# Performance work log

Hardware: AMD Instinct MI355X
Metric: run time of the kernel (lower is better)

Reference implementation:

```python
import jax, jax.numpy as jnp
import numpy as np

N, E, F_IN, HID, L, G = 50000, 800000, 128, 64, 3, 512
BN_EPS = 1e-5


def setup_inputs() -> dict:
    key = jax.random.key(0)
    ks = jax.random.split(key, 8)
    x = jax.random.normal(ks[0], (N, F_IN), dtype=jnp.float32)
    edge_index = jax.random.randint(ks[1], (2, E), 0, N, dtype=jnp.int32)
    batch = jnp.sort(jax.random.randint(ks[2], (N,), 0, G, dtype=jnp.int32))
    # params (Glorot-ish init for weights; BN init per module: gamma=1, beta=1e-4)
    W_feat = jax.random.normal(ks[3], (F_IN, HID), dtype=jnp.float32) / np.sqrt(F_IN)
    b_feat = jnp.zeros((HID,), jnp.float32)
    Ws = jax.random.normal(ks[4], (L, HID, HID), dtype=jnp.float32) / np.sqrt(HID)
    bs = jnp.zeros((L, HID), jnp.float32)
    bn_feat_g = jnp.ones((F_IN,), jnp.float32)
    bn_feat_b = jnp.full((F_IN,), 1e-4, jnp.float32)
    bn_g = jnp.ones((L, HID), jnp.float32)
    bn_b = jnp.full((L, HID), 1e-4, jnp.float32)
    return {"x": x, "edge_index": edge_index, "batch": batch,
            "bn_feat_g": bn_feat_g, "bn_feat_b": bn_feat_b,
            "W_feat": W_feat, "b_feat": b_feat,
            "bn_g": bn_g, "bn_b": bn_b, "Ws": Ws, "bs": bs}


def batch_norm(x, gamma, beta):
    # training-mode BatchNorm1d: biased variance over the node dimension
    mu = jnp.mean(x, axis=0)
    var = jnp.mean(jnp.square(x - mu), axis=0)
    return (x - mu) * jax.lax.rsqrt(var + BN_EPS) * gamma + beta


def gcn_conv(h, W, b, src, dst):
    # h: [N, d_in] -> linear then normalized gather-scatter with self-loops
    h = h @ W  # [N, d_out]
    n = h.shape[0]
    loop = jnp.arange(n, dtype=src.dtype)
    row = jnp.concatenate([src, loop])  # source (j)
    col = jnp.concatenate([dst, loop])  # target (i)
    w = jnp.ones(row.shape[0], h.dtype)
    deg = jax.ops.segment_sum(w, row, num_segments=n)  # PyG: deg over row
    dis = jnp.where(deg > 0, jax.lax.rsqrt(jnp.maximum(deg, 1.0)), 0.0)
    norm = dis[row] * w * dis[col]  # [E+N]
    out = jax.ops.segment_sum(norm[:, None] * h[row], col, num_segments=n)
    return out + b


def reference(x, edge_index, batch, bn_feat_g, bn_feat_b, W_feat, b_feat,
              bn_g, bn_b, Ws, bs):
    src, dst = edge_index[0], edge_index[1]
    h = batch_norm(x, bn_feat_g, bn_feat_b)
    h = jax.nn.relu(h @ W_feat + b_feat)  # conv_feat has gfn=True -> plain linear
    for i in range(L):
        h = batch_norm(h, bn_g[i], bn_b[i])
        h = jax.nn.relu(gcn_conv(h, Ws[i], bs[i], src, dst))
    graph_emb = jax.ops.segment_sum(h, batch, num_segments=G)  # global_add_pool
    return graph_emb
```

## Files before the change

kernel.cpp:

```cpp
#include <hip/hip_runtime.h>
#include <math.h>

#define HID 64
#define BN_EPS 1e-5f
#define NREP 64

typedef unsigned int uint;
typedef unsigned short ushort;


__device__ inline uint bf16pk(float a, float b) {
    uint ua = __builtin_bit_cast(uint, a);
    ua += 0x7fff + ((ua >> 16) & 1);
    uint ub = __builtin_bit_cast(uint, b);
    ub += 0x7fff + ((ub >> 16) & 1);
    return (ua >> 16) | (ub & 0xffff0000u);
}
__device__ inline float bfl(uint v) { return __builtin_bit_cast(float, v << 16); }
__device__ inline float bfh(uint v) { return __builtin_bit_cast(float, v & 0xffff0000u); }


__global__ __launch_bounds__(256) void k_hist_scan_stats(
        const int* __restrict__ ei, int E, int NB, int N, int HB,
        int* __restrict__ bcnt_d, int* __restrict__ bcnt_s, int* __restrict__ done,
        int* __restrict__ bbase_d, int* __restrict__ cursor_d,
        int* __restrict__ bbase_s, int* __restrict__ cursor_s,
        int* __restrict__ rowptr,
        const float* __restrict__ X, int n, float* __restrict__ stats) {
    __shared__ __align__(16) char smemraw[8192];
    __shared__ int lastFlag;
    int t = threadIdx.x;
    if ((int)blockIdx.x < HB) {
        int* hd = (int*)smemraw;
        int* hs = hd + 256;
        hd[t] = 0; hs[t] = 0;
        __syncthreads();
        for (int e = blockIdx.x * 256 + t; e < E; e += HB * 256) {
            int src = ei[e], dst = ei[E + e];
            atomicAdd(&hs[src >> 8], 1);
            atomicAdd(&hd[dst >> 8], 1);
        }
        __syncthreads();
        if (t < NB) {
            if (hd[t]) atomicAdd(&bcnt_d[t], hd[t]);
            if (hs[t]) atomicAdd(&bcnt_s[t], hs[t]);
        }
        __threadfence();
        __syncthreads();
        if (t == 0) lastFlag = (atomicAdd(done, 1) == HB - 1);
        __syncthreads();
        if (!lastFlag) return;
        int v = (t < NB) ? atomicAdd(&bcnt_d[t], 0) : 0;
        hd[t] = v; __syncthreads();
        for (int s = 1; s < 256; s <<= 1) { int u = (t >= s) ? hd[t - s] : 0; __syncthreads(); hd[t] += u; __syncthreads(); }
        int excl = hd[t] - v;
        if (t <= NB) bbase_d[t] = excl;
        if (t < NB) cursor_d[t] = excl;
        if (t == 0) rowptr[N] = E;
        __syncthreads();
        v = (t < NB) ? atomicAdd(&bcnt_s[t], 0) : 0;
        hs[t] = v; __syncthreads();
        for (int s = 1; s < 256; s <<= 1) { int u = (t >= s) ? hs[t - s] : 0; __syncthreads(); hs[t] += u; __syncthreads(); }
        excl = hs[t] - v;
        if (t <= NB) bbase_s[t] = excl;
        if (t < NB) cursor_s[t] = excl;
    } else {
        int b = blockIdx.x - HB;
        int SB = gridDim.x - HB;
        float4* shs = (float4*)smemraw;
        float4* shq = shs + 256;
        int c4 = t & 31, rsub = t >> 5;
        float4 s = make_float4(0.f, 0.f, 0.f, 0.f);
        float4 q = make_float4(0.f, 0.f, 0.f, 0.f);
        for (int r = b * 8 + rsub; r < n; r += SB * 8) {
            float4 v = ((const float4*)X)[(size_t)r * 32 + c4];
            s.x += v.x; s.y += v.y; s.z += v.z; s.w += v.w;
            q.x = fmaf(v.x, v.x, q.x); q.y = fmaf(v.y, v.y, q.y);
            q.z = fmaf(v.z, v.z, q.z); q.w = fmaf(v.w, v.w, q.w);
        }
        shs[t] = s; shq[t] = q;
        __syncthreads();
        if (rsub == 0) {
            #pragma unroll
            for (int k = 1; k < 8; k++) {
                float4 a = shs[t + k * 32], bq = shq[t + k * 32];
                s.x += a.x; s.y += a.y; s.z += a.z; s.w += a.w;
                q.x += bq.x; q.y += bq.y; q.z += bq.z; q.w += bq.w;
            }
            float* sb = stats + ((int)blockIdx.x & (NREP - 1)) * 256;
            atomicAdd(&sb[4 * t + 0], s.x); atomicAdd(&sb[4 * t + 1], s.y);
            atomicAdd(&sb[4 * t + 2], s.z); atomicAdd(&sb[4 * t + 3], s.w);
            atomicAdd(&sb[128 + 4 * t + 0], q.x); atomicAdd(&sb[128 + 4 * t + 1], q.y);
            atomicAdd(&sb[128 + 4 * t + 2], q.z); atomicAdd(&sb[128 + 4 * t + 3], q.w);
        }
    }
}


template <int K, bool RELU, bool DIS, bool STATS, bool HASB>
__device__ __forceinline__ void gemm_body(const float* __restrict__ X, const float* __restrict__ W,
                                          const float* __restrict__ stats,
                                          const float* __restrict__ gamma, const float* __restrict__ beta,
                                          const float* __restrict__ bias0, const float* __restrict__ dis,
                                          float n_inv, void* __restrict__ out, int n,
                                          float* __restrict__ sout, int bx) {
    constexpr int KC = 64;
    constexpr int XS = 68;
    __shared__ float Xs[KC * XS];
    __shared__ float Wsm[KC * HID];
    __shared__ float As[128], Cs[128];

    int t = threadIdx.x;
    int tx = t & 15, ty = t >> 4;
    int row0 = bx * 64;

    if (t < K) {
        float ssum = 0.f, qsum = 0.f;
        const float* sp = stats + t;
        #pragma unroll 8
        for (int r = 0; r < NREP; ++r) {
            ssum += sp[(size_t)r * 2 * K];
            qsum += sp[(size_t)r * 2 * K + K];
        }
        float mu = ssum * n_inv;
        float var = qsum * n_inv - mu * mu;
        float a = gamma[t] * rsqrtf(var + BN_EPS);
        As[t] = a;
        Cs[t] = beta[t] - mu * a;
    }
    __syncthreads();

    float acc[4][4];
    #pragma unroll
    for (int i = 0; i < 4; i++)
        #pragma unroll
        for (int j = 0; j < 4; j++) acc[i][j] = 0.f;
    float4 bp = make_float4(0.f, 0.f, 0.f, 0.f);

    for (int kc = 0; kc < K; kc += KC) {
        #pragma unroll
        for (int it = 0; it < 4; ++it) {
            int id = t + 256 * it;
            int r = id >> 4, c4 = id & 15;
            float4 v = make_float4(0.f, 0.f, 0.f, 0.f);
            if (row0 + r < n) v = *(const float4*)(X + (size_t)(row0 + r) * K + kc + 4 * c4);
            int kk = 4 * c4;
            Xs[(kk + 0) * XS + r] = v.x;
            Xs[(kk + 1) * XS + r] = v.y;
            Xs[(kk + 2) * XS + r] = v.z;
            Xs[(kk + 3) * XS + r] = v.w;
        }
        {
            const float4* wsrc = (const float4*)(W + (size_t)kc * HID);
            #pragma unroll
            for (int it = 0; it < 4; ++it) {
                int id = t + 256 * it;
                int kl = id >> 4;
                float4 raw = wsrc[id];
                float a = As[kc + kl], c = Cs[kc + kl];
                float4 sc;
                sc.x = a * raw.x; sc.y = a * raw.y; sc.z = a * raw.z; sc.w = a * raw.w;
                ((float4*)Wsm)[id] = sc;
                bp.x = fmaf(c, raw.x, bp.x);
                bp.y = fmaf(c, raw.y, bp.y);
                bp.z = fmaf(c, raw.z, bp.z);
                bp.w = fmaf(c, raw.w, bp.w);
            }
        }
        __syncthreads();
        #pragma unroll 8
        for (int k = 0; k < KC; ++k) {
            float4 xv = *(const float4*)&Xs[k * XS + 4 * ty];
            float4 wv = *(const float4*)&Wsm[k * HID + 4 * tx];
            acc[0][0] = fmaf(xv.x, wv.x, acc[0][0]);
            acc[0][1] = fmaf(xv.x, wv.y, acc[0][1]);
            acc[0][2] = fmaf(xv.x, wv.z, acc[0][2]);
            acc[0][3] = fmaf(xv.x, wv.w, acc[0][3]);
            acc[1][0] = fmaf(xv.y, wv.x, acc[1][0]);
            acc[1][1] = fmaf(xv.y, wv.y, acc[1][1]);
            acc[1][2] = fmaf(xv.y, wv.z, acc[1][2]);
            acc[1][3] = fmaf(xv.y, wv.w, acc[1][3]);
            acc[2][0] = fmaf(xv.z, wv.x, acc[2][0]);
            acc[2][1] = fmaf(xv.z, wv.y, acc[2][1]);
            acc[2][2] = fmaf(xv.z, wv.z, acc[2][2]);
            acc[2][3] = fmaf(xv.z, wv.w, acc[2][3]);
            acc[3][0] = fmaf(xv.w, wv.x, acc[3][0]);
            acc[3][1] = fmaf(xv.w, wv.y, acc[3][1]);
            acc[3][2] = fmaf(xv.w, wv.z, acc[3][2]);
            acc[3][3] = fmaf(xv.w, wv.w, acc[3][3]);
        }
        __syncthreads();
    }

    {
        float* redb = Xs + 2048;
        *(float4*)&redb[ty * 64 + 4 * tx] = bp;
        __syncthreads();
        if (t < 64) {
            float s = 0.f;
            #pragma unroll
            for (int k = 0; k < 16; ++k) s += redb[k * 64 + t];
            Xs[3072 + t] = s + (HASB ? bias0[t] : 0.f);
        }
        __syncthreads();
    }
    float4 bv = *(const float4*)&Xs[3072 + 4 * tx];

    float4 cs = make_float4(0.f, 0.f, 0.f, 0.f);
    float4 cq = make_float4(0.f, 0.f, 0.f, 0.f);
    #pragma unroll
    for (int i = 0; i < 4; ++i) {
        int row = row0 + 4 * ty + i;
        bool valid = row < n;
        float vx = acc[i][0] + bv.x, vy = acc[i][1] + bv.y;
        float vz = acc[i][2] + bv.z, vw = acc[i][3] + bv.w;
        if constexpr (DIS) {
            if (valid) {
                float d = dis[row];
                uint2 pk;
                pk.x = bf16pk(vx * d, vy * d);
                pk.y = bf16pk(vz * d, vw * d);
                *(uint2*)((ushort*)out + (size_t)row * HID + 4 * tx) = pk;
            }
        } else {
            float4 v;
            v.x = RELU ? fmaxf(vx, 0.f) : vx;
            v.y = RELU ? fmaxf(vy, 0.f) : vy;
            v.z = RELU ? fmaxf(vz, 0.f) : vz;
            v.w = RELU ? fmaxf(vw, 0.f) : vw;
            if (valid) {
                *(float4*)((float*)out + (size_t)row * HID + 4 * tx) = v;
                if constexpr (STATS) {
                    cs.x += v.x; cs.y += v.y; cs.z += v.z; cs.w += v.w;
                    cq.x = fmaf(v.x, v.x, cq.x); cq.y = fmaf(v.y, v.y, cq.y);
                    cq.z = fmaf(v.z, v.z, cq.z); cq.w = fmaf(v.w, v.w, cq.w);
                }
            }
        }
    }
    if constexpr (STATS) {
        __syncthreads();
        float* reds = Xs;
        float* redq = Xs + 1024;
        *(float4*)&reds[ty * 64 + 4 * tx] = cs;
        *(float4*)&redq[ty * 64 + 4 * tx] = cq;
        __syncthreads();
        if (t < 64) {
            float s = 0.f, q = 0.f;
            #pragma unroll
            for (int k = 0; k < 16; ++k) { s += reds[k * 64 + t]; q += redq[k * 64 + t]; }
            float* sb = sout + ((int)bx & (NREP - 1)) * 128;
            atomicAdd(&sb[t], s);
            atomicAdd(&sb[64 + t], q);
        }
    }
}

template <int K, bool RELU, bool DIS, bool STATS, bool HASB>
__global__ __launch_bounds__(256) void k_gemm(const float* __restrict__ X, const float* __restrict__ W,
                                              const float* __restrict__ stats,
                                              const float* __restrict__ gamma, const float* __restrict__ beta,
                                              const float* __restrict__ bias0, const float* __restrict__ dis,
                                              float n_inv, void* __restrict__ out, int n,
                                              float* __restrict__ sout) {
    gemm_body<K, RELU, DIS, STATS, HASB>(X, W, stats, gamma, beta, bias0, dis, n_inv, out, n, sout,
                                         (int)blockIdx.x);
}


__global__ __launch_bounds__(256) void k_scatter_gemm(
        const int* __restrict__ ei, int E, int NB, int SCB,
        int* __restrict__ cursor_d, int* __restrict__ cursor_s,
        uint* __restrict__ bedge, int* __restrict__ bsrc,
        const float* __restrict__ X, const float* __restrict__ W,
        const float* __restrict__ stats,
        const float* __restrict__ gamma, const float* __restrict__ beta,
        const float* __restrict__ bias0,
        float n_inv, void* __restrict__ out, int n, float* __restrict__ sout) {
    int t = threadIdx.x;
    if ((int)blockIdx.x < SCB) {
        __shared__ int hd[256], hs[256], curd[256], curs[256];
        int chunk = (E + SCB - 1) / SCB;
        int e0 = blockIdx.x * chunk;
        int e1 = min(e0 + chunk, E);
        if (t < NB) { hd[t] = 0; hs[t] = 0; }
        __syncthreads();
        for (int e = e0 + t; e < e1; e += 256) {
            int src = ei[e], dst = ei[E + e];
            atomicAdd(&hd[dst >> 8], 1);
            atomicAdd(&hs[src >> 8], 1);
        }
        __syncthreads();
        if (t < NB) {
            curd[t] = hd[t] ? atomicAdd(&cursor_d[t], hd[t]) : 0;
            curs[t] = hs[t] ? atomicAdd(&cursor_s[t], hs[t]) : 0;
        }
        __syncthreads();
        for (int e = e0 + t; e < e1; e += 256) {
            int src = ei[e], dst = ei[E + e];
            int pd = atomicAdd(&curd[dst >> 8], 1);
            bedge[pd] = ((uint)(dst & 255) << 16) | (uint)src;
            int ps = atomicAdd(&curs[src >> 8], 1);
            bsrc[ps] = src;
        }
    } else {
        gemm_body<128, true, false, true, true>(X, W, stats, gamma, beta, bias0, nullptr,
                                                n_inv, out, n, sout, (int)blockIdx.x - SCB);
    }
}


__global__ __launch_bounds__(256) void k_build_csr_outdeg(
        const uint* __restrict__ bedge, const int* __restrict__ bbase_d,
        const int* __restrict__ bsrc, const int* __restrict__ bbase_s,
        int N, int NB,
        int* __restrict__ rowptr, int* __restrict__ eidx, float* __restrict__ dis) {
    __shared__ int h[256], off[256], cur[256];
    int t = threadIdx.x, b = blockIdx.x;
    if (b < NB) {
        int base = bbase_d[b], end = bbase_d[b + 1];
        h[t] = 0; __syncthreads();
        for (int p = base + t; p < end; p += 256)
            atomicAdd(&h[(int)(bedge[p] >> 16) & 255], 1);
        __syncthreads();
        off[t] = h[t]; __syncthreads();
        for (int s = 1; s < 256; s <<= 1) { int u = (t >= s) ? off[t - s] : 0; __syncthreads(); off[t] += u; __syncthreads(); }
        int excl = off[t] - h[t];
        int node = (b << 8) + t;
        if (node <= N) rowptr[node] = base + excl;
        cur[t] = excl; __syncthreads();
        for (int p = base + t; p < end; p += 256) {
            uint be = bedge[p];
            int bin = (int)(be >> 16) & 255;
            int pos = atomicAdd(&cur[bin], 1);
            eidx[base + pos] = (int)(be & 0xffffu);
        }
    } else {
        int b2 = b - NB;
        int base = bbase_s[b2], end = bbase_s[b2 + 1];
        h[t] = 0; __syncthreads();
        for (int p = base + t; p < end; p += 256) atomicAdd(&h[bsrc[p] & 255], 1);
        __syncthreads();
        int node = (b2 << 8) + t;
        if (node < N) dis[node] = rsqrtf((float)(h[t] + 1));
    }
}


template <bool POOL>
__global__ __launch_bounds__(256) void k_agg(const ushort* __restrict__ s, const int* __restrict__ rowptr,
                                             const int* __restrict__ eidx, const float* __restrict__ dis,
                                             const float* __restrict__ bias, float* __restrict__ out, int n,
                                             float* __restrict__ sout, const int* __restrict__ batch,
                                             float* __restrict__ pool_out) {
    __shared__ float shs[8 * 64];
    __shared__ float shq[8 * 64];
    __shared__ int ib[8];
    int t = threadIdx.x;
    int nl = t >> 5;
    int li = t & 31;
    int slot = li >> 3;
    int c = li & 7;
    int i = blockIdx.x * 8 + nl;
    const uint4* sp4 = (const uint4*)s;
    float a[8];
    #pragma unroll
    for (int k = 0; k < 8; ++k) a[k] = 0.f;
    bool valid = i < n;
    if (valid) {
        int qe = rowptr[i + 1];
        int q = rowptr[i] + slot;
        while (q < qe) {
            int qm = qe - 1;
            int q1 = q + 4, q2 = q + 8, q3 = q + 12;
            bool p1 = q1 < qe, p2 = q2 < qe, p3 = q3 < qe;
            int j0 = eidx[q];
            int j1 = eidx[min(q1, qm)];
            int j2 = eidx[min(q2, qm)];
            int j3 = eidx[min(q3, qm)];
            if (!p1) j1 = i;
            if (!p2) j2 = i;
            if (!p3) j3 = i;
            uint4 v0 = sp4[(size_t)j0 * 8 + c];
            uint4 v1 = sp4[(size_t)j1 * 8 + c];
            uint4 v2 = sp4[(size_t)j2 * 8 + c];
            uint4 v3 = sp4[(size_t)j3 * 8 + c];
            float m1 = p1 ? 1.f : 0.f;
            float m2 = p2 ? 1.f : 0.f;
            float m3 = p3 ? 1.f : 0.f;
            q += 16;
            a[0] += bfl(v0.x); a[1] += bfh(v0.x);
            a[2] += bfl(v0.y); a[3] += bfh(v0.y);
            a[4] += bfl(v0.z); a[5] += bfh(v0.z);
            a[6] += bfl(v0.w); a[7] += bfh(v0.w);
            a[0] = fmaf(m1, bfl(v1.x), a[0]); a[1] = fmaf(m1, bfh(v1.x), a[1]);
            a[2] = fmaf(m1, bfl(v1.y), a[2]); a[3] = fmaf(m1, bfh(v1.y), a[3]);
            a[4] = fmaf(m1, bfl(v1.z), a[4]); a[5] = fmaf(m1, bfh(v1.z), a[5]);
            a[6] = fmaf(m1, bfl(v1.w), a[6]); a[7] = fmaf(m1, bfh(v1.w), a[7]);
            a[0] = fmaf(m2, bfl(v2.x), a[0]); a[1] = fmaf(m2, bfh(v2.x), a[1]);
            a[2] = fmaf(m2, bfl(v2.y), a[2]); a[3] = fmaf(m2, bfh(v2.y), a[3]);
            a[4] = fmaf(m2, bfl(v2.z), a[4]); a[5] = fmaf(m2, bfh(v2.z), a[5]);
            a[6] = fmaf(m2, bfl(v2.w), a[6]); a[7] = fmaf(m2, bfh(v2.w), a[7]);
            a[0] = fmaf(m3, bfl(v3.x), a[0]); a[1] = fmaf(m3, bfh(v3.x), a[1]);
            a[2] = fmaf(m3, bfl(v3.y), a[2]); a[3] = fmaf(m3, bfh(v3.y), a[3]);
            a[4] = fmaf(m3, bfl(v3.z), a[4]); a[5] = fmaf(m3, bfh(v3.z), a[5]);
            a[6] = fmaf(m3, bfl(v3.w), a[6]); a[7] = fmaf(m3, bfh(v3.w), a[7]);
        }
    }
    #pragma unroll
    for (int k = 0; k < 8; ++k) a[k] += __shfl_xor(a[k], 8);
    #pragma unroll
    for (int k = 0; k < 8; ++k) a[k] += __shfl_xor(a[k], 16);

    if (li < 8) {
        float r[8];
        if (valid) {
            uint4 v = sp4[(size_t)i * 8 + c];
            a[0] += bfl(v.x); a[1] += bfh(v.x);
            a[2] += bfl(v.y); a[3] += bfh(v.y);
            a[4] += bfl(v.z); a[5] += bfh(v.z);
            a[6] += bfl(v.w); a[7] += bfh(v.w);
            float d = dis[i];
            float4 b0 = *(const float4*)(bias + 8 * c);
            float4 b1 = *(const float4*)(bias + 8 * c + 4);
            r[0] = fmaxf(fmaf(d, a[0], b0.x), 0.f);
            r[1] = fmaxf(fmaf(d, a[1], b0.y), 0.f);
            r[2] = fmaxf(fmaf(d, a[2], b0.z), 0.f);
            r[3] = fmaxf(fmaf(d, a[3], b0.w), 0.f);
            r[4] = fmaxf(fmaf(d, a[4], b1.x), 0.f);
            r[5] = fmaxf(fmaf(d, a[5], b1.y), 0.f);
            r[6] = fmaxf(fmaf(d, a[6], b1.z), 0.f);
            r[7] = fmaxf(fmaf(d, a[7], b1.w), 0.f);
            if constexpr (!POOL) {
                *(float4*)(out + (size_t)i * HID + 8 * c)     = make_float4(r[0], r[1], r[2], r[3]);
                *(float4*)(out + (size_t)i * HID + 8 * c + 4) = make_float4(r[4], r[5], r[6], r[7]);
            }
        } else {
            #pragma unroll
            for (int k = 0; k < 8; ++k) r[k] = 0.f;
        }
        #pragma unroll
        for (int k = 0; k < 8; ++k) shs[nl * 64 + 8 * c + k] = r[k];
        if constexpr (!POOL) {
            #pragma unroll
            for (int k = 0; k < 8; ++k) shq[nl * 64 + 8 * c + k] = r[k] * r[k];
        }
    }
    if constexpr (POOL) {
        if (li == 0) ib[nl] = valid ? batch[i] : -1;
    }
    __syncthreads();
    if (t < 64) {
        if constexpr (!POOL) {
            float ss = 0.f, qq = 0.f;
            #pragma unroll
            for (int k = 0; k < 8; ++k) { ss += shs[k * 64 + t]; qq += shq[k * 64 + t]; }
            float* sb = sout + ((int)blockIdx.x & (NREP - 1)) * 128;
            atomicAdd(&sb[t], ss);
            atomicAdd(&sb[64 + t], qq);
        } else {
            int g = ib[0];
            float run = shs[t];
            #pragma unroll
            for (int k = 1; k < 8; ++k) {
                int gk = ib[k];
                float v = shs[k * 64 + t];
                if (gk == g) {
                    run += v;
                } else {
                    if (g >= 0) atomicAdd(&pool_out[(size_t)g * HID + t], run);
                    g = gk; run = v;
                }
            }
            if (g >= 0) atomicAdd(&pool_out[(size_t)g * HID + t], run);
        }
    }
}


extern "C" void kernel_launch(void* const* d_in, const int* in_sizes, int n_in,
                              void* d_out, int out_size, void* d_ws, size_t ws_size,
                              hipStream_t stream) {
    const float* x     = (const float*)d_in[0];
    const int*   ei    = (const int*)d_in[1];
    const int*   batch = (const int*)d_in[2];
    const float* bnfg  = (const float*)d_in[3];
    const float* bnfb  = (const float*)d_in[4];
    const float* Wfeat = (const float*)d_in[5];
    const float* bfeat = (const float*)d_in[6];
    const float* bng   = (const float*)d_in[7];
    const float* bnb   = (const float*)d_in[8];
    const float* Ws    = (const float*)d_in[9];
    const float* bs    = (const float*)d_in[10];
    float* out = (float*)d_out;

    const int N   = in_sizes[2];
    const int E   = in_sizes[1] / 2;
    const int L   = in_sizes[9] / (HID * HID);
    const int NB  = (N + 255) >> 8;
    const int HB  = 128;
    const int SB  = 512;
    const int SCB = 256;
    const int gG  = (N + 63) / 64;
    const int gA  = (N + 7) / 8;
    const float n_inv = 1.f / (float)N;

    char* w = (char*)d_ws;
    auto alloc = [&](size_t bytes) { char* p = w; w += (bytes + 255) & ~(size_t)255; return p; };
    int*   bcnt_d = (int*)alloc(256 * 4);
    int*   bcnt_s = (int*)alloc(256 * 4);
    int*   done   = (int*)alloc(256);
    float* statsX = (float*)alloc((size_t)NREP * 256 * 4);
    float* statsL = (float*)alloc((size_t)3 * NREP * 128 * 4);
    size_t zero_bytes = (size_t)(w - (char*)d_ws);
    int*   bbase_d  = (int*)alloc(257 * 4);
    int*   cursor_d = (int*)alloc(256 * 4);
    int*   bbase_s  = (int*)alloc(257 * 4);
    int*   cursor_s = (int*)alloc(256 * 4);
    int*   rowptr   = (int*)alloc(((size_t)N + 1) * 4);
    int*   eidx     = (int*)alloc((size_t)E * 4);
    float* dis      = (float*)alloc((size_t)N * 4);
    float* bufA     = (float*)alloc((size_t)N * HID * 4);
    ushort* bufB    = (ushort*)alloc((size_t)N * HID * 2);
    uint*  bedge    = (uint*)alloc((size_t)E * 4);
    int*   bsrc     = (int*)alloc((size_t)E * 4);

    hipMemsetAsync(d_ws, 0, zero_bytes, stream);
    hipMemsetAsync(d_out, 0, (size_t)out_size * sizeof(float), stream);

    k_hist_scan_stats<<<HB + SB, 256, 0, stream>>>(ei, E, NB, N, HB, bcnt_d, bcnt_s, done,
                                                   bbase_d, cursor_d, bbase_s, cursor_s, rowptr,
                                                   x, N, statsX);
    k_scatter_gemm<<<SCB + gG, 256, 0, stream>>>(ei, E, NB, SCB, cursor_d, cursor_s, bedge, bsrc,
                                                 x, Wfeat, statsX, bnfg, bnfb, bfeat,
                                                 n_inv, (void*)bufA, N, statsL);
    k_build_csr_outdeg<<<2 * NB, 256, 0, stream>>>(bedge, bbase_d, bsrc, bbase_s, N, NB,
                                                   rowptr, eidx, dis);

    for (int l = 0; l < L; ++l) {
        k_gemm<64, false, true, false, false><<<gG, 256, 0, stream>>>(
            bufA, Ws + (size_t)l * HID * HID, statsL + (size_t)l * NREP * 128,
            bng + (size_t)l * HID, bnb + (size_t)l * HID,
            nullptr, dis, n_inv, (void*)bufB, N, nullptr);
        if (l < L - 1) {
            k_agg<false><<<gA, 256, 0, stream>>>(bufB, rowptr, eidx, dis, bs + (size_t)l * HID,
                                                 bufA, N, statsL + (size_t)(l + 1) * NREP * 128,
                                                 nullptr, nullptr);
        } else {
            k_agg<true><<<gA, 256, 0, stream>>>(bufB, rowptr, eidx, dis, bs + (size_t)l * HID,
                                                nullptr, N, nullptr, batch, out);
        }
    }
}
```

Measured before the change: 260.4 us.

## Fuse CSR fill with first-layer GEMM and parallelize BN stats reduction

Splits the out-degree computation into its own kernel and merges the CSR fill with the layer-0 GEMM in one launch, so the two independent pieces of work run as different block ranges of the same grid. It also spreads the per-feature BN stat reduction across all 256 threads with a shared-memory combine step, where previously only K threads did it. The aim is to cut one serialized launch boundary and shorten the stats prologue of every GEMM, at the cost of an extra small kernel and a barrier.

After: 251.4 us. 1.04x faster.

```diff
diff --git a/kernel.cpp b/kernel.cpp
--- a/kernel.cpp
+++ b/kernel.cpp
@@ -106,6 +106,7 @@
                                           float* __restrict__ sout, int bx) {
     constexpr int KC = 64;
     constexpr int XS = 68;
+    constexpr int NSUB = 256 / K;
     __shared__ float Xs[KC * XS];
     __shared__ float Wsm[KC * HID];
     __shared__ float As[128], Cs[128];
@@ -114,16 +115,26 @@
     int tx = t & 15, ty = t >> 4;
     int row0 = bx * 64;
 
-    if (t < K) {
+    {
+        int f = t & (K - 1);
+        int sub = t / K;
         float ssum = 0.f, qsum = 0.f;
-        const float* sp = stats + t;
-        #pragma unroll 8
-        for (int r = 0; r < NREP; ++r) {
+        const float* sp = stats + f;
+        #pragma unroll 4
+        for (int r = sub; r < NREP; r += NSUB) {
             ssum += sp[(size_t)r * 2 * K];
             qsum += sp[(size_t)r * 2 * K + K];
         }
-        float mu = ssum * n_inv;
-        float var = qsum * n_inv - mu * mu;
+        Xs[t] = ssum;
+        Xs[256 + t] = qsum;
+    }
+    __syncthreads();
+    if (t < K) {
+        float ss = 0.f, qq = 0.f;
+        #pragma unroll
+        for (int s = 0; s < NSUB; ++s) { ss += Xs[s * K + t]; qq += Xs[256 + s * K + t]; }
+        float mu = ss * n_inv;
+        float var = qq * n_inv - mu * mu;
         float a = gamma[t] * rsqrtf(var + BN_EPS);
         As[t] = a;
         Cs[t] = beta[t] - mu * a;
@@ -249,7 +260,7 @@
             float s = 0.f, q = 0.f;
             #pragma unroll
             for (int k = 0; k < 16; ++k) { s += reds[k * 64 + t]; q += redq[k * 64 + t]; }
-            float* sb = sout + ((int)bx & (NREP - 1)) * 128;
+            float* sb = sout + (bx & (NREP - 1)) * 128;
             atomicAdd(&sb[t], s);
             atomicAdd(&sb[64 + t], q);
         }
@@ -310,14 +321,30 @@
 }
 
 
-__global__ __launch_bounds__(256) void k_build_csr_outdeg(
-        const uint* __restrict__ bedge, const int* __restrict__ bbase_d,
-        const int* __restrict__ bsrc, const int* __restrict__ bbase_s,
-        int N, int NB,
-        int* __restrict__ rowptr, int* __restrict__ eidx, float* __restrict__ dis) {
-    __shared__ int h[256], off[256], cur[256];
+__global__ __launch_bounds__(256) void k_dis(const int* __restrict__ bsrc, const int* __restrict__ bbase_s,
+                                             int N, float* __restrict__ dis) {
+    __shared__ int h[256];
+    int t = threadIdx.x, b = blockIdx.x;
+    int base = bbase_s[b], end = bbase_s[b + 1];
+    h[t] = 0; __syncthreads();
+    for (int p = base + t; p < end; p += 256) atomicAdd(&h[bsrc[p] & 255], 1);
+    __syncthreads();
+    int node = (b << 8) + t;
+    if (node < N) dis[node] = rsqrtf((float)(h[t] + 1));
+}
+
+
+__global__ __launch_bounds__(256) void k_fill_gemm(
+        const uint* __restrict__ bedge, const int* __restrict__ bbase_d, int N, int NB,
+        int* __restrict__ rowptr, int* __restrict__ eidx,
+        const float* __restrict__ X, const float* __restrict__ W,
+        const float* __restrict__ stats,
+        const float* __restrict__ gamma, const float* __restrict__ beta,
+        const float* __restrict__ dis,
+        float n_inv, void* __restrict__ out, int n) {
     int t = threadIdx.x, b = blockIdx.x;
     if (b < NB) {
+        __shared__ int h[256], off[256], cur[256];
         int base = bbase_d[b], end = bbase_d[b + 1];
         h[t] = 0; __syncthreads();
         for (int p = base + t; p < end; p += 256)
@@ -336,13 +363,8 @@
             eidx[base + pos] = (int)(be & 0xffffu);
         }
     } else {
-        int b2 = b - NB;
-        int base = bbase_s[b2], end = bbase_s[b2 + 1];
-        h[t] = 0; __syncthreads();
-        for (int p = base + t; p < end; p += 256) atomicAdd(&h[bsrc[p] & 255], 1);
-        __syncthreads();
-        int node = (b2 << 8) + t;
-        if (node < N) dis[node] = rsqrtf((float)(h[t] + 1));
+        gemm_body<64, false, true, false, false>(X, W, stats, gamma, beta, nullptr, dis,
+                                                 n_inv, out, n, nullptr, b - NB);
     }
 }
 
@@ -534,10 +556,15 @@
     k_scatter_gemm<<<SCB + gG, 256, 0, stream>>>(ei, E, NB, SCB, cursor_d, cursor_s, bedge, bsrc,
                                                  x, Wfeat, statsX, bnfg, bnfb, bfeat,
                                                  n_inv, (void*)bufA, N, statsL);
-    k_build_csr_outdeg<<<2 * NB, 256, 0, stream>>>(bedge, bbase_d, bsrc, bbase_s, N, NB,
-                                                   rowptr, eidx, dis);
-
-    for (int l = 0; l < L; ++l) {
+    k_dis<<<NB, 256, 0, stream>>>(bsrc, bbase_s, N, dis);
+    k_fill_gemm<<<NB + gG, 256, 0, stream>>>(bedge, bbase_d, N, NB, rowptr, eidx,
+                                             bufA, Ws, statsL, bng, bnb, dis,
+                                             n_inv, (void*)bufB, N);
+    k_agg<false><<<gA, 256, 0, stream>>>(bufB, rowptr, eidx, dis, bs,
+                                         bufA, N, statsL + (size_t)1 * NREP * 128,
+                                         nullptr, nullptr);
+
+    for (int l = 1; l < L; ++l) {
         k_gemm<64, false, true, false, false><<<gG, 256, 0, stream>>>(
             bufA, Ws + (size_t)l * HID * HID, statsL + (size_t)l * NREP * 128,
             bng + (size_t)l * HID, bnb + (size_t)l * HID,
```
